# Performance work log

Measured on AMD Instinct MI355X. Metric: run time of the kernel, lower is better.

The kernel has to match this reference:

```python
import jax, jax.numpy as jnp
import numpy as np

N_EMBD = 2048
N_HEAD = 16
HEAD_DIM = N_EMBD // N_HEAD
BATCH = 2
SEQ = 2048


def setup_inputs() -> dict:
    key = jax.random.key(0)
    k1, k2, k3 = jax.random.split(key, 3)
    scale = 0.02
    return {
        "hidden_states": jax.random.normal(k1, (BATCH, SEQ, N_EMBD), dtype=jnp.float32),
        "c_attn_w": jax.random.normal(k2, (N_EMBD, 3 * N_EMBD), dtype=jnp.float32) * scale,
        "c_attn_b": jnp.zeros((3 * N_EMBD,), dtype=jnp.float32),
        "c_proj_w": jax.random.normal(k3, (N_EMBD, N_EMBD), dtype=jnp.float32) * scale,
        "c_proj_b": jnp.zeros((N_EMBD,), dtype=jnp.float32),
    }


def reference(hidden_states, c_attn_w, c_attn_b, c_proj_w, c_proj_b):
    B, S, E = hidden_states.shape
    # Fused QKV projection (Conv1D: x @ W + b)
    qkv = hidden_states @ c_attn_w + c_attn_b  # [B, S, 3E]
    q, k, v = jnp.split(qkv, 3, axis=-1)
    # split heads -> [B, H, S, D]
    def split_heads(t):
        return t.reshape(B, S, N_HEAD, HEAD_DIM).transpose(0, 2, 1, 3)
    q, k, v = split_heads(q), split_heads(k), split_heads(v)
    # scaled scores, causal mask, softmax (dropout p=0 -> identity)
    scores = jnp.einsum("bhqd,bhkd->bhqk", q, k) / jnp.asarray(
        HEAD_DIM ** 0.5, dtype=q.dtype)
    causal = jnp.tril(jnp.ones((S, S), dtype=bool))  # [S, S]
    mask_value = jnp.finfo(scores.dtype).min
    scores = jnp.where(causal[None, None, :, :], scores, mask_value)
    attn = jax.nn.softmax(scores, axis=-1)
    out = jnp.einsum("bhqk,bhkd->bhqd", attn, v)  # [B, H, S, D]
    # merge heads -> [B, S, E]
    out = out.transpose(0, 2, 1, 3).reshape(B, S, E)
    # output projection
    return out @ c_proj_w + c_proj_b
```

## Files before the change

kernel.cpp:

```cpp
#include <hip/hip_runtime.h>
#include <hip/hip_bf16.h>

typedef __bf16 bf16x8 __attribute__((ext_vector_type(8)));
typedef float f32x4 __attribute__((ext_vector_type(4)));

__device__ __forceinline__ float bf2f(unsigned short u) {
  union { unsigned int i; float f; } v; v.i = ((unsigned int)u) << 16; return v.f;
}
__device__ __forceinline__ unsigned short f2bf(float f) {
  union { unsigned int i; float f; } v; v.f = f;
  unsigned int i = v.i;
  return (unsigned short)((i + 0x7FFFu + ((i >> 16) & 1u)) >> 16);
}

typedef const __attribute__((address_space(1))) unsigned int* gas_ptr;
typedef __attribute__((address_space(3))) unsigned int* las_ptr;
__device__ __forceinline__ void gload_lds16(const unsigned short* g, unsigned short* l) {
  __builtin_amdgcn_global_load_lds((gas_ptr)(const void*)g, (las_ptr)(void*)l, 16, 0, 0);
}

__global__ __launch_bounds__(256) void detect_k(const unsigned short* __restrict__ h,
                                                int* __restrict__ flag) {
  __shared__ int s[256];
  int cnt = 0;
  for (int i = threadIdx.x; i < 4096; i += 256) {
    unsigned short u = h[2 * i];
    int e = (u >> 7) & 0xFF;
    if ((e >= 96 && e <= 140) || u == 0) cnt++;
  }
  s[threadIdx.x] = cnt;
  __syncthreads();
  for (int o = 128; o > 0; o >>= 1) {
    if (threadIdx.x < o) s[threadIdx.x] += s[threadIdx.x + o];
    __syncthreads();
  }
  if (threadIdx.x == 0) *flag = (s[0] >= 3600) ? 1 : 0;
}

__global__ __launch_bounds__(256) void cvt_hidden_k(const void* __restrict__ src,
                                                    unsigned short* __restrict__ dst, int n,
                                                    const int* __restrict__ flag) {
  if (*flag) return;
  for (int i = blockIdx.x * 256 + threadIdx.x; i < n; i += gridDim.x * 256)
    dst[i] = f2bf(((const float*)src)[i]);
}

__global__ __launch_bounds__(256) void transpose_w2_k(const void* __restrict__ w_qkv,
                                                      const void* __restrict__ w_proj,
                                                      unsigned short* __restrict__ dst_qkv,
                                                      unsigned short* __restrict__ dst_proj,
                                                      const int* __restrict__ flag) {
  __shared__ unsigned short tile[32][33];
  const int f = *flag;
  int bid = blockIdx.x;
  const void* src;
  unsigned short* dst;
  int R = 2048, C, cx, cy;
  if (bid < 12288) {
    src = w_qkv; dst = dst_qkv; C = 6144; cx = bid % 192; cy = bid / 192;
  } else {
    bid -= 12288;
    src = w_proj; dst = dst_proj; C = 2048; cx = bid % 64; cy = bid / 64;
  }
  const int x = threadIdx.x & 31;
  const int y = threadIdx.x >> 5;
  const int r0 = cy * 32, c0 = cx * 32;
#pragma unroll
  for (int i = 0; i < 4; i++) {
    size_t idx = (size_t)(r0 + y + 8 * i) * C + c0 + x;
    tile[y + 8 * i][x] = f ? ((const unsigned short*)src)[idx]
                           : f2bf(((const float*)src)[idx]);
  }
  __syncthreads();
#pragma unroll
  for (int i = 0; i < 4; i++)
    dst[(size_t)(c0 + y + 8 * i) * R + r0 + x] = tile[x][y + 8 * i];
}

__global__ __launch_bounds__(256) void transpose_v_k(const unsigned short* __restrict__ qkv,
                                                     unsigned short* __restrict__ Vt) {
  __shared__ unsigned short tile[32][33];
  const int bh = blockIdx.z;
  const int b = bh >> 4, hh = bh & 15;
  const int s0 = blockIdx.x * 32, d0 = blockIdx.y * 32;
  const int x = threadIdx.x & 31, y = threadIdx.x >> 5;
#pragma unroll
  for (int i = 0; i < 4; i++)
    tile[y + 8 * i][x] =
        qkv[((size_t)b * 2048 + s0 + y + 8 * i) * 6144 + 4096 + hh * 128 + d0 + x];
  __syncthreads();
#pragma unroll
  for (int i = 0; i < 4; i++)
    Vt[((size_t)bh * 128 + d0 + y + 8 * i) * 2048 + s0 + x] = tile[x][y + 8 * i];
}

__global__ __launch_bounds__(512, 2) void gemm_qkv_k(const unsigned short* __restrict__ A_bf,
                                                     const unsigned short* __restrict__ A_cvt,
                                                     const unsigned short* __restrict__ Bt,
                                                     const void* __restrict__ bias,
                                                     unsigned short* __restrict__ Cout,
                                                     int M, int N, int K,
                                                     const int* __restrict__ flag) {
  __shared__ __attribute__((aligned(16))) unsigned short As[2][256][64];
  __shared__ __attribute__((aligned(16))) unsigned short Bs[2][192][64];
  const int f = *flag;
  const unsigned short* Ap = f ? A_bf : A_cvt;
  const int t = threadIdx.x;
  const int wave = t >> 6, lane = t & 63;
  const int col = lane & 15, quad = lane >> 4;
  const int wm = wave >> 1, wn = wave & 1;

  const int nbx = N / 192;
  int wgid = blockIdx.y * nbx + blockIdx.x;
  const int nwg = (M >> 8) * nbx;
  if ((nwg & 7) == 0) {
    const int cpx = nwg >> 3;
    wgid = (wgid & 7) * cpx + (wgid >> 3);
  }
  const int n0 = (wgid % nbx) * 192;
  const int m0 = (wgid / nbx) << 8;

  const int srow = lane >> 3;
  const int sx = ((lane & 7) ^ srow) * 8;
  const int rsw = col & 7;

  const unsigned short* pA = Ap + (size_t)(m0 + wave * 8 + srow) * K + sx;
  const unsigned short* pB = Bt + (size_t)(n0 + wave * 8 + srow) * K + sx;
  const int NT = K >> 6;

#define STAGE_A(d, q, kt) \
  gload_lds16(pA + (size_t)((q) * 64) * K + (size_t)(kt) * 64, &As[(d)][(q) * 64 + wave * 8][0])
#define STAGE_B(d, q, kt) \
  gload_lds16(pB + (size_t)((q) * 64) * K + (size_t)(kt) * 64, &Bs[(d)][(q) * 64 + wave * 8][0])
#define LDA(d, rf, kk) \
  (*(const bf16x8*)&As[(d)][wm * 64 + (rf) * 16 + col][((((kk) << 2) | quad) ^ rsw) * 8])
#define LDB(d, cf, kk) \
  (*(const bf16x8*)&Bs[(d)][wn * 96 + (cf) * 16 + col][((((kk) << 2) | quad) ^ rsw) * 8])

  const f32x4 fzero = {0.f, 0.f, 0.f, 0.f};
  f32x4 acc[4][6];
#pragma unroll
  for (int i = 0; i < 4; i++)
#pragma unroll
    for (int j = 0; j < 6; j++) acc[i][j] = fzero;

  bf16x8 aA[4][2], aB[4][2];

  STAGE_A(0, 0, 0); STAGE_A(0, 1, 0); STAGE_A(0, 2, 0); STAGE_A(0, 3, 0);
  STAGE_B(0, 0, 0); STAGE_B(0, 1, 0); STAGE_B(0, 2, 0);
  STAGE_A(1, 0, 1); STAGE_A(1, 1, 1); STAGE_A(1, 2, 1); STAGE_A(1, 3, 1);
  asm volatile("s_waitcnt vmcnt(4)" ::: "memory");
  __builtin_amdgcn_sched_barrier(0);
  __builtin_amdgcn_s_barrier();

#define BODY(D, U, FIRST, SB, SA, VM2, VM3, PRER, ACUR, ANXT)                              \
  {                                                                                        \
                                            \
    if (FIRST) {                                                                           \
      _Pragma("unroll") for (int rf = 0; rf < 4; rf++) {                                   \
        ACUR[rf][0] = LDA(D, rf, 0);                                                       \
        ACUR[rf][1] = LDA(D, rf, 1);                                                       \
      }                                                                                    \
    }                                                                                      \
    bf16x8 b01[2][2];                                                                      \
    _Pragma("unroll") for (int c = 0; c < 2; c++) {                                        \
      b01[c][0] = LDB(D, c, 0);                                                            \
      b01[c][1] = LDB(D, c, 1);                                                            \
    }                                                                                      \
    if (SB) { STAGE_B((D) ^ 1, 0, (U) + 1); STAGE_B((D) ^ 1, 1, (U) + 1); }                \
    __builtin_amdgcn_s_barrier();                                                          \
    asm volatile("s_waitcnt lgkmcnt(0)" ::: "memory");                                     \
    __builtin_amdgcn_sched_barrier(0);                                                     \
    __builtin_amdgcn_s_setprio(1);                                                         \
    _Pragma("unroll") for (int rf = 0; rf < 4; rf++)                                       \
      _Pragma("unroll") for (int c = 0; c < 2; c++) {                                      \
        acc[rf][c] = __builtin_amdgcn_mfma_f32_16x16x32_bf16(ACUR[rf][0], b01[c][0], acc[rf][c], 0, 0, 0); \
        acc[rf][c] = __builtin_amdgcn_mfma_f32_16x16x32_bf16(ACUR[rf][1], b01[c][1], acc[rf][c], 0, 0, 0); \
      }                                                                                    \
    __builtin_amdgcn_s_setprio(0);                                                         \
                                            \
    bf16x8 b23[2][2];                                                                      \
    _Pragma("unroll") for (int c = 0; c < 2; c++) {                                        \
      b23[c][0] = LDB(D, (c) + 2, 0);                                                      \
      b23[c][1] = LDB(D, (c) + 2, 1);                                                      \
    }                                                                                      \
    if (SB) STAGE_B((D) ^ 1, 2, (U) + 1);                                                  \
    if (SA) { STAGE_A(D, 0, (U) + 2); STAGE_A(D, 1, (U) + 2); }                            \
    asm volatile("s_waitcnt " VM2 ::: "memory");                                           \
    __builtin_amdgcn_s_barrier();                                                          \
    asm volatile("s_waitcnt lgkmcnt(0)" ::: "memory");                                     \
    __builtin_amdgcn_sched_barrier(0);                                                     \
    __builtin_amdgcn_s_setprio(1);                                                         \
    _Pragma("unroll") for (int rf = 0; rf < 4; rf++)                                       \
      _Pragma("unroll") for (int c = 0; c < 2; c++) {                                      \
        acc[rf][(c) + 2] = __builtin_amdgcn_mfma_f32_16x16x32_bf16(ACUR[rf][0], b23[c][0], acc[rf][(c) + 2], 0, 0, 0); \
        acc[rf][(c) + 2] = __builtin_amdgcn_mfma_f32_16x16x32_bf16(ACUR[rf][1], b23[c][1], acc[rf][(c) + 2], 0, 0, 0); \
      }                                                                                    \
    __builtin_amdgcn_s_setprio(0);                                                         \
                                            \
    bf16x8 b45[2][2];                                                                      \
    _Pragma("unroll") for (int c = 0; c < 2; c++) {                                        \
      b45[c][0] = LDB(D, (c) + 4, 0);                                                      \
      b45[c][1] = LDB(D, (c) + 4, 1);                                                      \
    }                                                                                      \
    __builtin_amdgcn_sched_barrier(0);  \
    if (PRER) {                                                                            \
      _Pragma("unroll") for (int rf = 0; rf < 4; rf++) {                                   \
        ANXT[rf][0] = LDA((D) ^ 1, rf, 0);                                                 \
        ANXT[rf][1] = LDA((D) ^ 1, rf, 1);                                                 \
      }                                                                                    \
    }                                                                                      \
    if (SA) { STAGE_A(D, 2, (U) + 2); STAGE_A(D, 3, (U) + 2); }                            \
    asm volatile("s_waitcnt " VM3 ::: "memory");                                           \
    __builtin_amdgcn_s_barrier();                                                          \
    if (PRER) asm volatile("s_waitcnt lgkmcnt(8)" ::: "memory");                           \
    else      asm volatile("s_waitcnt lgkmcnt(0)" ::: "memory");                           \
    __builtin_amdgcn_sched_barrier(0);                                                     \
    __builtin_amdgcn_s_setprio(1);                                                         \
    _Pragma("unroll") for (int rf = 0; rf < 4; rf++)                                       \
      _Pragma("unroll") for (int c = 0; c < 2; c++) {                                      \
        acc[rf][(c) + 4] = __builtin_amdgcn_mfma_f32_16x16x32_bf16(ACUR[rf][0], b45[c][0], acc[rf][(c) + 4], 0, 0, 0); \
        acc[rf][(c) + 4] = __builtin_amdgcn_mfma_f32_16x16x32_bf16(ACUR[rf][1], b45[c][1], acc[rf][(c) + 4], 0, 0, 0); \
      }                                                                                    \
    __builtin_amdgcn_s_setprio(0);                                                         \
  }

  BODY(0, 0, 1, 1, 1, "vmcnt(5)", "vmcnt(4)", 1, aA, aB)
  BODY(1, 1, 0, 1, 1, "vmcnt(5)", "vmcnt(4)", 1, aB, aA)
  for (int u2 = 2; u2 + 3 < NT; u2 += 2) {
    BODY(0, u2, 0, 1, 1, "vmcnt(5)", "vmcnt(4)", 1, aA, aB)
    BODY(1, u2 + 1, 0, 1, 1, "vmcnt(5)", "vmcnt(4)", 1, aB, aA)
  }
  BODY(0, NT - 2, 0, 1, 0, "vmcnt(3)", "vmcnt(0)", 1, aA, aB)
  BODY(1, NT - 1, 0, 0, 0, "vmcnt(0)", "vmcnt(0)", 0, aB, aA)

#undef BODY
#undef STAGE_A
#undef STAGE_B
#undef LDA
#undef LDB

#pragma unroll
  for (int cf = 0; cf < 6; cf++) {
    int n = n0 + wn * 96 + cf * 16 + col;
    float bv = f ? bf2f(((const unsigned short*)bias)[n]) : ((const float*)bias)[n];
#pragma unroll
    for (int rf = 0; rf < 4; rf++)
#pragma unroll
      for (int r = 0; r < 4; r++) {
        int m = m0 + wm * 64 + rf * 16 + quad * 4 + r;
        Cout[(size_t)m * N + n] = f2bf(acc[rf][cf][r] + bv);
      }
  }
}

__global__ __launch_bounds__(256) void gemm_bias_k(const unsigned short* __restrict__ A_bf,
                                                   const unsigned short* __restrict__ A_cvt,
                                                   const unsigned short* __restrict__ Bt,
                                                   const void* __restrict__ bias,
                                                   void* __restrict__ Cout,
                                                   int M, int N, int K,
                                                   const int* __restrict__ flag,
                                                   int final_out) {
  __shared__ __attribute__((aligned(16))) unsigned short As[128][64];
  __shared__ __attribute__((aligned(16))) unsigned short Bs[128][64];
  const int f = *flag;
  const unsigned short* A = f ? A_bf : A_cvt;
  const int t = threadIdx.x;
  const int wave = t >> 6, lane = t & 63;
  const int col = lane & 15, quad = lane >> 4;
  const int wm = wave >> 1, wn = wave & 1;
  const int m0 = blockIdx.y * 128, n0 = blockIdx.x * 128;
  const int srow = lane >> 3;
  const int schunk = ((lane & 7) ^ srow) * 8;
  const int rsw = col & 7;

  const f32x4 fzero = {0.f, 0.f, 0.f, 0.f};
  f32x4 acc[4][4];
#pragma unroll
  for (int i = 0; i < 4; i++)
#pragma unroll
    for (int j = 0; j < 4; j++) acc[i][j] = fzero;

  for (int k0 = 0; k0 < K; k0 += 64) {
    __syncthreads();
#pragma unroll
    for (int c = 0; c < 4; c++) {
      int seg = wave * 4 + c;
      int row = seg * 8 + srow;
      gload_lds16(&A [(size_t)(m0 + row) * K + k0 + schunk], &As[seg * 8][0]);
      gload_lds16(&Bt[(size_t)(n0 + row) * K + k0 + schunk], &Bs[seg * 8][0]);
    }
    __syncthreads();
#pragma unroll
    for (int ks = 0; ks < 2; ks++) {
      bf16x8 af[4], bfr[4];
#pragma unroll
      for (int i = 0; i < 4; i++)
        af[i] = *(const bf16x8*)&As[wm * 64 + i * 16 + col][(((ks << 2) | quad) ^ rsw) * 8];
#pragma unroll
      for (int j = 0; j < 4; j++)
        bfr[j] = *(const bf16x8*)&Bs[wn * 64 + j * 16 + col][(((ks << 2) | quad) ^ rsw) * 8];
#pragma unroll
      for (int i = 0; i < 4; i++)
#pragma unroll
        for (int j = 0; j < 4; j++)
          acc[i][j] = __builtin_amdgcn_mfma_f32_16x16x32_bf16(af[i], bfr[j], acc[i][j], 0, 0, 0);
    }
  }
  const int f32o = final_out ? (f == 0) : 0;
#pragma unroll
  for (int j = 0; j < 4; j++) {
    int n = n0 + wn * 64 + j * 16 + col;
    float bv = f ? bf2f(((const unsigned short*)bias)[n]) : ((const float*)bias)[n];
#pragma unroll
    for (int i = 0; i < 4; i++)
#pragma unroll
      for (int r = 0; r < 4; r++) {
        int m = m0 + wm * 64 + i * 16 + quad * 4 + r;
        float v = acc[i][j][r] + bv;
        if (f32o) ((float*)Cout)[(size_t)m * N + n] = v;
        else      ((unsigned short*)Cout)[(size_t)m * N + n] = f2bf(v);
      }
  }
}

#define ATT_SCALE 0.08838834764831845f
__global__ __launch_bounds__(256) void attn_k(const unsigned short* __restrict__ qkv,
                                              const unsigned short* __restrict__ Vt,
                                              unsigned short* __restrict__ O) {
  __shared__ __attribute__((aligned(16))) unsigned short Ks[64][136];
  __shared__ __attribute__((aligned(16))) unsigned short Vs[128][72];
  __shared__ __attribute__((aligned(16))) unsigned short Ps[4][16][72];
  const int t = threadIdx.x;
  const int wave = t >> 6, lane = t & 63;
  const int col = lane & 15, quad = lane >> 4;
  const int h = blockIdx.y, b = blockIdx.z;
  const size_t base = (size_t)b * 2048 * 6144;
  const size_t vbase = ((size_t)(b * 16 + h)) * 128 * 2048;
  const int hcol = h * 128;

  const int kr = t >> 2;
  const int kc = (t & 3) * 8;
  const int vr = t >> 1;
  const int vc = (t & 1) * 32;

  const f32x4 fzero = {0.f, 0.f, 0.f, 0.f};

  for (int pass = 0; pass < 2; pass++) {
    const int qt = pass ? (int)blockIdx.x : 31 - (int)blockIdx.x;

    bf16x8 qf[4];
    {
      size_t qrow = base + (size_t)(qt * 64 + wave * 16 + col) * 6144 + hcol;
#pragma unroll
      for (int ks = 0; ks < 4; ks++)
        qf[ks] = *(const bf16x8*)&qkv[qrow + ks * 32 + quad * 8];
    }

    f32x4 o[8];
#pragma unroll
    for (int i = 0; i < 8; i++) o[i] = fzero;
    float l_i[4] = {0.f, 0.f, 0.f, 0.f};

    __syncthreads();
    {
      size_t grow = base + (size_t)kr * 6144 + 2048 + hcol;
#pragma unroll
      for (int p = 0; p < 4; p++)
        *(bf16x8*)&Ks[kr][kc + p * 32] = *(const bf16x8*)&qkv[grow + kc + p * 32];
      size_t vrow = vbase + (size_t)vr * 2048;
#pragma unroll
      for (int c = 0; c < 4; c++)
        *(bf16x8*)&Vs[vr][vc + c * 8] = *(const bf16x8*)&Vt[vrow + vc + c * 8];
    }
    __syncthreads();

    for (int kt = 0; kt <= qt; kt++) {
      bf16x8 kreg[4], vreg[4];
      const bool pf = (kt < qt);
      if (pf) {
        size_t grow = base + (size_t)((kt + 1) * 64 + kr) * 6144 + 2048 + hcol;
#pragma unroll
        for (int p = 0; p < 4; p++)
          kreg[p] = *(const bf16x8*)&qkv[grow + kc + p * 32];
        size_t vrow = vbase + (size_t)vr * 2048 + (kt + 1) * 64;
#pragma unroll
        for (int c = 0; c < 4; c++)
          vreg[c] = *(const bf16x8*)&Vt[vrow + vc + c * 8];
      }

      f32x4 sc[4];
#pragma unroll
      for (int nb = 0; nb < 4; nb++) {
        f32x4 s = fzero;
#pragma unroll
        for (int ks = 0; ks < 4; ks++) {
          bf16x8 kf = *(const bf16x8*)&Ks[nb * 16 + col][ks * 32 + quad * 8];
          s = __builtin_amdgcn_mfma_f32_16x16x32_bf16(qf[ks], kf, s, 0, 0, 0);
        }
        sc[nb] = s;
      }

      const bool diag = (kt == qt);
#pragma unroll
      for (int nb = 0; nb < 4; nb++) {
        int kl = nb * 16 + col;
#pragma unroll
        for (int r = 0; r < 4; r++) {
          float s = sc[nb][r];
          if (diag && kl > wave * 16 + quad * 4 + r) s = -1e30f;
          float p = __expf(s * ATT_SCALE);
          l_i[r] += p;
          Ps[wave][quad * 4 + r][nb * 16 + col] = f2bf(p);
        }
      }
      bf16x8 pfr[2];
#pragma unroll
      for (int ks2 = 0; ks2 < 2; ks2++)
        pfr[ks2] = *(const bf16x8*)&Ps[wave][col][ks2 * 32 + quad * 8];
#pragma unroll
      for (int nbo = 0; nbo < 8; nbo++)
#pragma unroll
        for (int ks2 = 0; ks2 < 2; ks2++) {
          bf16x8 vf = *(const bf16x8*)&Vs[nbo * 16 + col][ks2 * 32 + quad * 8];
          o[nbo] = __builtin_amdgcn_mfma_f32_16x16x32_bf16(pfr[ks2], vf, o[nbo], 0, 0, 0);
        }

      __syncthreads();
      if (pf) {
#pragma unroll
        for (int p = 0; p < 4; p++)
          *(bf16x8*)&Ks[kr][kc + p * 32] = kreg[p];
#pragma unroll
        for (int c = 0; c < 4; c++)
          *(bf16x8*)&Vs[vr][vc + c * 8] = vreg[c];
      }
      __syncthreads();
    }

#pragma unroll
    for (int r = 0; r < 4; r++) {
#pragma unroll
      for (int off = 1; off < 16; off <<= 1)
        l_i[r] += __shfl_xor(l_i[r], off, 64);
      l_i[r] = 1.0f / l_i[r];
    }

#pragma unroll
    for (int nbo = 0; nbo < 8; nbo++)
#pragma unroll
      for (int r = 0; r < 4; r++) {
        int m = qt * 64 + wave * 16 + quad * 4 + r;
        O[((size_t)b * 2048 + m) * 2048 + hcol + nbo * 16 + col] = f2bf(o[nbo][r] * l_i[r]);
      }
  }
}

extern "C" void kernel_launch(void* const* d_in, const int* in_sizes, int n_in,
                              void* d_out, int out_size, void* d_ws, size_t ws_size,
                              hipStream_t stream) {
  (void)in_sizes; (void)n_in; (void)out_size; (void)ws_size;
  int* flag = (int*)d_ws;
  unsigned short* wsu = (unsigned short*)d_ws + 128;
  unsigned short* Wt_qkv    = wsu;
  unsigned short* Wt_proj   = Wt_qkv + (size_t)6144 * 2048;
  unsigned short* QKV       = Wt_proj + (size_t)2048 * 2048;
  unsigned short* hidden_bf = QKV + (size_t)4096 * 6144;
  unsigned short* Obuf      = Wt_qkv;
  unsigned short* Vt        = hidden_bf + (size_t)4096 * 2048;

  detect_k<<<1, 256, 0, stream>>>((const unsigned short*)d_in[0], flag);
  cvt_hidden_k<<<2048, 256, 0, stream>>>(d_in[0], hidden_bf, 4096 * 2048, flag);
  transpose_w2_k<<<16384, 256, 0, stream>>>(d_in[1], d_in[3], Wt_qkv, Wt_proj, flag);
  gemm_qkv_k<<<dim3(32, 16), 512, 0, stream>>>((const unsigned short*)d_in[0], hidden_bf,
                                               Wt_qkv, d_in[2], QKV,
                                               4096, 6144, 2048, flag);
  transpose_v_k<<<dim3(64, 4, 32), 256, 0, stream>>>(QKV, Vt);
  attn_k<<<dim3(16, 16, 2), 256, 0, stream>>>(QKV, Vt, Obuf);
  gemm_bias_k<<<dim3(16, 32), 256, 0, stream>>>(Obuf, Obuf, Wt_proj, d_in[4], d_out,
                                                4096, 2048, 2048, flag, 1);
}
```

Measured before the change: 389.1 us.

## Pipeline projection GEMM, vectorize conversion and transpose stores, raise MFMA priority

Replaces the simple projection GEMM with a 512-thread, 256x128-tile kernel that double-buffers A and B in LDS. It also remaps workgroups for L2 locality and uses explicit waitcnt and barrier scheduling, as the QKV GEMM already does. It vectorizes the fp32-to-bf16 hidden conversion to eight elements per thread and widens the weight-transpose stores to four-element vectors. It also wraps the attention MFMA blocks in setprio hints. The new GEMM raises register and LDS pressure, and its hand-tuned vmcnt/lgkmcnt counts must match the issued loads exactly.

```diff
diff --git a/kernel.cpp b/kernel.cpp
--- a/kernel.cpp
+++ b/kernel.cpp
@@ -3,6 +3,8 @@
 
 typedef __bf16 bf16x8 __attribute__((ext_vector_type(8)));
 typedef float f32x4 __attribute__((ext_vector_type(4)));
+typedef unsigned short us4 __attribute__((ext_vector_type(4)));
+typedef unsigned short us8 __attribute__((ext_vector_type(8)));
 
 __device__ __forceinline__ float bf2f(unsigned short u) {
   union { unsigned int i; float f; } v; v.i = ((unsigned int)u) << 16; return v.f;
@@ -38,11 +40,17 @@
 }
 
 __global__ __launch_bounds__(256) void cvt_hidden_k(const void* __restrict__ src,
-                                                    unsigned short* __restrict__ dst, int n,
+                                                    unsigned short* __restrict__ dst, int n8,
                                                     const int* __restrict__ flag) {
   if (*flag) return;
-  for (int i = blockIdx.x * 256 + threadIdx.x; i < n; i += gridDim.x * 256)
-    dst[i] = f2bf(((const float*)src)[i]);
+  const float4* s = (const float4*)src;
+  for (int i = blockIdx.x * 256 + threadIdx.x; i < n8; i += gridDim.x * 256) {
+    float4 a = s[2 * i], b = s[2 * i + 1];
+    us8 o;
+    o[0] = f2bf(a.x); o[1] = f2bf(a.y); o[2] = f2bf(a.z); o[3] = f2bf(a.w);
+    o[4] = f2bf(b.x); o[5] = f2bf(b.y); o[6] = f2bf(b.z); o[7] = f2bf(b.w);
+    *(us8*)&dst[8 * i] = o;
+  }
 }
 
 __global__ __launch_bounds__(256) void transpose_w2_k(const void* __restrict__ w_qkv,
@@ -72,9 +80,12 @@
                            : f2bf(((const float*)src)[idx]);
   }
   __syncthreads();
-#pragma unroll
-  for (int i = 0; i < 4; i++)
-    dst[(size_t)(c0 + y + 8 * i) * R + r0 + x] = tile[x][y + 8 * i];
+  const int orow = threadIdx.x >> 3;
+  const int oc = (threadIdx.x & 7) * 4;
+  us4 v;
+  v[0] = tile[oc][orow]; v[1] = tile[oc + 1][orow];
+  v[2] = tile[oc + 2][orow]; v[3] = tile[oc + 3][orow];
+  *(us4*)&dst[(size_t)(c0 + orow) * R + r0 + oc] = v;
 }
 
 __global__ __launch_bounds__(256) void transpose_v_k(const unsigned short* __restrict__ qkv,
@@ -155,7 +166,6 @@
 
 #define BODY(D, U, FIRST, SB, SA, VM2, VM3, PRER, ACUR, ANXT)                              \
   {                                                                                        \
-                                            \
     if (FIRST) {                                                                           \
       _Pragma("unroll") for (int rf = 0; rf < 4; rf++) {                                   \
         ACUR[rf][0] = LDA(D, rf, 0);                                                       \
@@ -178,7 +188,6 @@
         acc[rf][c] = __builtin_amdgcn_mfma_f32_16x16x32_bf16(ACUR[rf][1], b01[c][1], acc[rf][c], 0, 0, 0); \
       }                                                                                    \
     __builtin_amdgcn_s_setprio(0);                                                         \
-                                            \
     bf16x8 b23[2][2];                                                                      \
     _Pragma("unroll") for (int c = 0; c < 2; c++) {                                        \
       b23[c][0] = LDB(D, (c) + 2, 0);                                                      \
@@ -197,7 +206,6 @@
         acc[rf][(c) + 2] = __builtin_amdgcn_mfma_f32_16x16x32_bf16(ACUR[rf][1], b23[c][1], acc[rf][(c) + 2], 0, 0, 0); \
       }                                                                                    \
     __builtin_amdgcn_s_setprio(0);                                                         \
-                                            \
     bf16x8 b45[2][2];                                                                      \
     _Pragma("unroll") for (int c = 0; c < 2; c++) {                                        \
       b45[c][0] = LDB(D, (c) + 4, 0);                                                      \
@@ -254,26 +262,46 @@
   }
 }
 
-__global__ __launch_bounds__(256) void gemm_bias_k(const unsigned short* __restrict__ A_bf,
-                                                   const unsigned short* __restrict__ A_cvt,
-                                                   const unsigned short* __restrict__ Bt,
-                                                   const void* __restrict__ bias,
-                                                   void* __restrict__ Cout,
-                                                   int M, int N, int K,
-                                                   const int* __restrict__ flag,
-                                                   int final_out) {
-  __shared__ __attribute__((aligned(16))) unsigned short As[128][64];
-  __shared__ __attribute__((aligned(16))) unsigned short Bs[128][64];
+__global__ __launch_bounds__(512, 2) void gemm_proj_k(const unsigned short* __restrict__ A,
+                                                      const unsigned short* __restrict__ Bt,
+                                                      const void* __restrict__ bias,
+                                                      void* __restrict__ Cout,
+                                                      int M, int N, int K,
+                                                      const int* __restrict__ flag) {
+  __shared__ __attribute__((aligned(16))) unsigned short As[2][256][64];
+  __shared__ __attribute__((aligned(16))) unsigned short Bs[2][128][64];
   const int f = *flag;
-  const unsigned short* A = f ? A_bf : A_cvt;
   const int t = threadIdx.x;
   const int wave = t >> 6, lane = t & 63;
   const int col = lane & 15, quad = lane >> 4;
   const int wm = wave >> 1, wn = wave & 1;
-  const int m0 = blockIdx.y * 128, n0 = blockIdx.x * 128;
+
+  const int nbx = N >> 7;
+  int wgid = blockIdx.y * nbx + blockIdx.x;
+  const int nwg = (M >> 8) * nbx;
+  if ((nwg & 7) == 0) {
+    const int cpx = nwg >> 3;
+    wgid = (wgid & 7) * cpx + (wgid >> 3);
+  }
+  const int n0 = (wgid % nbx) << 7;
+  const int m0 = (wgid / nbx) << 8;
+
   const int srow = lane >> 3;
-  const int schunk = ((lane & 7) ^ srow) * 8;
+  const int sx = ((lane & 7) ^ srow) * 8;
   const int rsw = col & 7;
+
+  const unsigned short* pA = A + (size_t)(m0 + wave * 8 + srow) * K + sx;
+  const unsigned short* pB = Bt + (size_t)(n0 + wave * 8 + srow) * K + sx;
+  const int NT = K >> 6;
+
+#define STAGE_A(d, q, kt) \
+  gload_lds16(pA + (size_t)((q) * 64) * K + (size_t)(kt) * 64, &As[(d)][(q) * 64 + wave * 8][0])
+#define STAGE_B(d, q, kt) \
+  gload_lds16(pB + (size_t)((q) * 64) * K + (size_t)(kt) * 64, &Bs[(d)][(q) * 64 + wave * 8][0])
+#define LDA(d, rf, kk) \
+  (*(const bf16x8*)&As[(d)][wm * 64 + (rf) * 16 + col][((((kk) << 2) | quad) ^ rsw) * 8])
+#define LDB(d, cf, kk) \
+  (*(const bf16x8*)&Bs[(d)][wn * 64 + (cf) * 16 + col][((((kk) << 2) | quad) ^ rsw) * 8])
 
   const f32x4 fzero = {0.f, 0.f, 0.f, 0.f};
   f32x4 acc[4][4];
@@ -282,43 +310,94 @@
 #pragma unroll
     for (int j = 0; j < 4; j++) acc[i][j] = fzero;
 
-  for (int k0 = 0; k0 < K; k0 += 64) {
-    __syncthreads();
-#pragma unroll
-    for (int c = 0; c < 4; c++) {
-      int seg = wave * 4 + c;
-      int row = seg * 8 + srow;
-      gload_lds16(&A [(size_t)(m0 + row) * K + k0 + schunk], &As[seg * 8][0]);
-      gload_lds16(&Bt[(size_t)(n0 + row) * K + k0 + schunk], &Bs[seg * 8][0]);
-    }
-    __syncthreads();
-#pragma unroll
-    for (int ks = 0; ks < 2; ks++) {
-      bf16x8 af[4], bfr[4];
-#pragma unroll
-      for (int i = 0; i < 4; i++)
-        af[i] = *(const bf16x8*)&As[wm * 64 + i * 16 + col][(((ks << 2) | quad) ^ rsw) * 8];
-#pragma unroll
-      for (int j = 0; j < 4; j++)
-        bfr[j] = *(const bf16x8*)&Bs[wn * 64 + j * 16 + col][(((ks << 2) | quad) ^ rsw) * 8];
-#pragma unroll
-      for (int i = 0; i < 4; i++)
-#pragma unroll
-        for (int j = 0; j < 4; j++)
-          acc[i][j] = __builtin_amdgcn_mfma_f32_16x16x32_bf16(af[i], bfr[j], acc[i][j], 0, 0, 0);
-    }
-  }
-  const int f32o = final_out ? (f == 0) : 0;
-#pragma unroll
-  for (int j = 0; j < 4; j++) {
-    int n = n0 + wn * 64 + j * 16 + col;
+  bf16x8 aA[4][2], aB[4][2];
+
+  STAGE_A(0, 0, 0); STAGE_A(0, 1, 0); STAGE_A(0, 2, 0); STAGE_A(0, 3, 0);
+  STAGE_B(0, 0, 0); STAGE_B(0, 1, 0);
+  STAGE_A(1, 0, 1); STAGE_A(1, 1, 1); STAGE_A(1, 2, 1); STAGE_A(1, 3, 1);
+  asm volatile("s_waitcnt vmcnt(4)" ::: "memory");
+  __builtin_amdgcn_sched_barrier(0);
+  __builtin_amdgcn_s_barrier();
+
+#define BODY(D, U, FIRST, SB, SA, VM1, VM2, PRER, ACUR, ANXT)                              \
+  {                                                                                        \
+    if (FIRST) {                                                                           \
+      _Pragma("unroll") for (int rf = 0; rf < 4; rf++) {                                   \
+        ACUR[rf][0] = LDA(D, rf, 0);                                                       \
+        ACUR[rf][1] = LDA(D, rf, 1);                                                       \
+      }                                                                                    \
+    }                                                                                      \
+    bf16x8 b01[2][2];                                                                      \
+    _Pragma("unroll") for (int c = 0; c < 2; c++) {                                        \
+      b01[c][0] = LDB(D, c, 0);                                                            \
+      b01[c][1] = LDB(D, c, 1);                                                            \
+    }                                                                                      \
+    if (SB) { STAGE_B((D) ^ 1, 0, (U) + 1); STAGE_B((D) ^ 1, 1, (U) + 1); }                \
+    asm volatile("s_waitcnt " VM1 ::: "memory");                                           \
+    __builtin_amdgcn_s_barrier();                                                          \
+    asm volatile("s_waitcnt lgkmcnt(0)" ::: "memory");                                     \
+    __builtin_amdgcn_sched_barrier(0);                                                     \
+    __builtin_amdgcn_s_setprio(1);                                                         \
+    _Pragma("unroll") for (int rf = 0; rf < 4; rf++)                                       \
+      _Pragma("unroll") for (int c = 0; c < 2; c++) {                                      \
+        acc[rf][c] = __builtin_amdgcn_mfma_f32_16x16x32_bf16(ACUR[rf][0], b01[c][0], acc[rf][c], 0, 0, 0); \
+        acc[rf][c] = __builtin_amdgcn_mfma_f32_16x16x32_bf16(ACUR[rf][1], b01[c][1], acc[rf][c], 0, 0, 0); \
+      }                                                                                    \
+    __builtin_amdgcn_s_setprio(0);                                                         \
+    bf16x8 b23[2][2];                                                                      \
+    _Pragma("unroll") for (int c = 0; c < 2; c++) {                                        \
+      b23[c][0] = LDB(D, (c) + 2, 0);                                                      \
+      b23[c][1] = LDB(D, (c) + 2, 1);                                                      \
+    }                                                                                      \
+    __builtin_amdgcn_sched_barrier(0);                      \
+    if (PRER) {                                                                            \
+      _Pragma("unroll") for (int rf = 0; rf < 4; rf++) {                                   \
+        ANXT[rf][0] = LDA((D) ^ 1, rf, 0);                                                 \
+        ANXT[rf][1] = LDA((D) ^ 1, rf, 1);                                                 \
+      }                                                                                    \
+    }                                                                                      \
+    if (SA) { STAGE_A(D, 0, (U) + 2); STAGE_A(D, 1, (U) + 2);                              \
+              STAGE_A(D, 2, (U) + 2); STAGE_A(D, 3, (U) + 2); }                            \
+    asm volatile("s_waitcnt " VM2 ::: "memory");                                           \
+    __builtin_amdgcn_s_barrier();                                                          \
+    if (PRER) asm volatile("s_waitcnt lgkmcnt(8)" ::: "memory");                           \
+    else      asm volatile("s_waitcnt lgkmcnt(0)" ::: "memory");                           \
+    __builtin_amdgcn_sched_barrier(0);                                                     \
+    __builtin_amdgcn_s_setprio(1);                                                         \
+    _Pragma("unroll") for (int rf = 0; rf < 4; rf++)                                       \
+      _Pragma("unroll") for (int c = 0; c < 2; c++) {                                      \
+        acc[rf][(c) + 2] = __builtin_amdgcn_mfma_f32_16x16x32_bf16(ACUR[rf][0], b23[c][0], acc[rf][(c) + 2], 0, 0, 0); \
+        acc[rf][(c) + 2] = __builtin_amdgcn_mfma_f32_16x16x32_bf16(ACUR[rf][1], b23[c][1], acc[rf][(c) + 2], 0, 0, 0); \
+      }                                                                                    \
+    __builtin_amdgcn_s_setprio(0);                                                         \
+  }
+
+  BODY(0, 0, 1, 1, 1, "vmcnt(2)", "vmcnt(4)", 1, aA, aB)
+  BODY(1, 1, 0, 1, 1, "vmcnt(2)", "vmcnt(4)", 1, aB, aA)
+  for (int u2 = 2; u2 + 3 < NT; u2 += 2) {
+    BODY(0, u2, 0, 1, 1, "vmcnt(2)", "vmcnt(4)", 1, aA, aB)
+    BODY(1, u2 + 1, 0, 1, 1, "vmcnt(2)", "vmcnt(4)", 1, aB, aA)
+  }
+  BODY(0, NT - 2, 0, 1, 0, "vmcnt(2)", "vmcnt(0)", 1, aA, aB)
+  BODY(1, NT - 1, 0, 0, 0, "vmcnt(0)", "vmcnt(0)", 0, aB, aA)
+
+#undef BODY
+#undef STAGE_A
+#undef STAGE_B
+#undef LDA
+#undef LDB
+
+  const int f32o = (f == 0);
+#pragma unroll
+  for (int cf = 0; cf < 4; cf++) {
+    int n = n0 + wn * 64 + cf * 16 + col;
     float bv = f ? bf2f(((const unsigned short*)bias)[n]) : ((const float*)bias)[n];
 #pragma unroll
-    for (int i = 0; i < 4; i++)
+    for (int rf = 0; rf < 4; rf++)
 #pragma unroll
       for (int r = 0; r < 4; r++) {
-        int m = m0 + wm * 64 + i * 16 + quad * 4 + r;
-        float v = acc[i][j][r] + bv;
+        int m = m0 + wm * 64 + rf * 16 + quad * 4 + r;
+        float v = acc[rf][cf][r] + bv;
         if (f32o) ((float*)Cout)[(size_t)m * N + n] = v;
         else      ((unsigned short*)Cout)[(size_t)m * N + n] = f2bf(v);
       }
@@ -391,6 +470,7 @@
       }
 
       f32x4 sc[4];
+      __builtin_amdgcn_s_setprio(1);
 #pragma unroll
       for (int nb = 0; nb < 4; nb++) {
         f32x4 s = fzero;
@@ -401,6 +481,7 @@
         }
         sc[nb] = s;
       }
+      __builtin_amdgcn_s_setprio(0);
 
       const bool diag = (kt == qt);
 #pragma unroll
@@ -419,6 +500,7 @@
 #pragma unroll
       for (int ks2 = 0; ks2 < 2; ks2++)
         pfr[ks2] = *(const bf16x8*)&Ps[wave][col][ks2 * 32 + quad * 8];
+      __builtin_amdgcn_s_setprio(1);
 #pragma unroll
       for (int nbo = 0; nbo < 8; nbo++)
 #pragma unroll
@@ -426,6 +508,7 @@
           bf16x8 vf = *(const bf16x8*)&Vs[nbo * 16 + col][ks2 * 32 + quad * 8];
           o[nbo] = __builtin_amdgcn_mfma_f32_16x16x32_bf16(pfr[ks2], vf, o[nbo], 0, 0, 0);
         }
+      __builtin_amdgcn_s_setprio(0);
 
       __syncthreads();
       if (pf) {
@@ -471,13 +554,13 @@
   unsigned short* Vt        = hidden_bf + (size_t)4096 * 2048;
 
   detect_k<<<1, 256, 0, stream>>>((const unsigned short*)d_in[0], flag);
-  cvt_hidden_k<<<2048, 256, 0, stream>>>(d_in[0], hidden_bf, 4096 * 2048, flag);
+  cvt_hidden_k<<<2048, 256, 0, stream>>>(d_in[0], hidden_bf, (4096 * 2048) / 8, flag);
   transpose_w2_k<<<16384, 256, 0, stream>>>(d_in[1], d_in[3], Wt_qkv, Wt_proj, flag);
   gemm_qkv_k<<<dim3(32, 16), 512, 0, stream>>>((const unsigned short*)d_in[0], hidden_bf,
                                                Wt_qkv, d_in[2], QKV,
                                                4096, 6144, 2048, flag);
   transpose_v_k<<<dim3(64, 4, 32), 256, 0, stream>>>(QKV, Vt);
   attn_k<<<dim3(16, 16, 2), 256, 0, stream>>>(QKV, Vt, Obuf);
-  gemm_bias_k<<<dim3(16, 32), 256, 0, stream>>>(Obuf, Obuf, Wt_proj, d_in[4], d_out,
-                                                4096, 2048, 2048, flag, 1);
-}
+  gemm_proj_k<<<dim3(16, 16), 512, 0, stream>>>(Obuf, Wt_proj, d_in[4], d_out,
+                                                4096, 2048, 2048, flag);
+}
```

Measured after the change: 385.0 us. Within noise of the previous version (-1.1%).
